# Kernel optimization log

Measured on AMD Instinct MI355X. Metric: run time of the kernel, lower is better.

## Reference

```python
import jax, jax.numpy as jnp
import numpy as np

KS = 3            # kernel_size
DILS = (1, 2, 4)  # dilation_list == padding_list
EPS = 1e-5        # BN eps


def _unfold3(x, d):
    # emulate F.unfold(kernel=3, dilation=d, padding=d, stride=1).view(b, c, 9, h, w)
    b, c, h, w = x.shape
    xp = jnp.pad(x, ((0, 0), (0, 0), (d, d), (d, d)))
    pats = [xp[:, :, i * d:i * d + h, j * d:j * d + w] for i in range(KS) for j in range(KS)]
    return jnp.stack(pats, axis=2)


def _conv1x1(x, w, b):
    return jnp.einsum('bchw,oc->bohw', x, w) + b[None, :, None, None]


def _bn_relu(x, g, be, m, v):
    s = g / jnp.sqrt(v + EPS)
    return jax.nn.relu(x * s[None, :, None, None] + (be - m * s)[None, :, None, None])


def _proj(x, w1, b1, g1, be1, m1, v1, w2, b2, g2, be2, m2, v2):
    h = _bn_relu(_conv1x1(x, w1, b1), g1, be1, m1, v1)
    return _bn_relu(_conv1x1(h, w2, b2), g2, be2, m2, v2)


def setup_inputs():
    key = jax.random.key(0)
    Cin, Ck, Cv, Cout = 512, 256, 256, 512
    B, H, W = 4, 64, 64
    ks = iter(jax.random.split(key, 48))

    def nrm(shape, s=0.02):
        return jax.random.normal(next(ks), shape, jnp.float32) * s

    def bn(c):
        return (jnp.ones((c,), jnp.float32) + nrm((c,), 0.1),  # gamma
                nrm((c,), 0.1),                                 # beta
                nrm((c,), 0.1),                                 # running mean
                jax.random.uniform(next(ks), (c,), jnp.float32, 0.5, 1.5))  # running var

    inp = {"x": jax.random.normal(next(ks), (B, Cin, H, W), jnp.float32)}
    for p in ("k", "q"):
        g1, be1, m1, v1 = bn(Ck)
        g2, be2, m2, v2 = bn(Ck)
        inp.update({
            p + "1_w": nrm((Ck, Cin)), p + "1_b": nrm((Ck,)),
            p + "1_g": g1, p + "1_be": be1, p + "1_m": m1, p + "1_v": v1,
            p + "2_w": nrm((Ck, Ck)), p + "2_b": nrm((Ck,)),
            p + "2_g": g2, p + "2_be": be2, p + "2_m": m2, p + "2_v": v2,
        })
    inp["v_w"] = nrm((Cv, Cin)); inp["v_b"] = nrm((Cv,))
    inp["w_w"] = nrm((Cout, Cv)); inp["w_b"] = nrm((Cout,))
    return inp


def reference(x,
              k1_w, k1_b, k1_g, k1_be, k1_m, k1_v,
              k2_w, k2_b, k2_g, k2_be, k2_m, k2_v,
              q1_w, q1_b, q1_g, q1_be, q1_m, q1_v,
              q2_w, q2_b, q2_g, q2_be, q2_m, q2_v,
              v_w, v_b, w_w, w_b):
    # scale == 1: MaxPool2d(1x1-equivalent) and final bilinear resize are identities.
    value = _conv1x1(x, v_w, v_b)                                  # (b,cv,h,w)
    keyf = _proj(x, k1_w, k1_b, k1_g, k1_be, k1_m, k1_v,
                 k2_w, k2_b, k2_g, k2_be, k2_m, k2_v)              # (b,ck,h,w)
    query = _proj(x, q1_w, q1_b, q1_g, q1_be, q1_m, q1_v,
                  q2_w, q2_b, q2_g, q2_be, q2_m, q2_v)             # (b,ck,h,w)
    uk = jnp.concatenate([_unfold3(keyf, d) for d in DILS], axis=2)   # (b,ck,27,h,w)
    uv = jnp.concatenate([_unfold3(value, d) for d in DILS], axis=2)  # (b,cv,27,h,w)
    sim = jnp.sum(uk * query[:, :, None], axis=1, keepdims=True)      # (b,1,27,h,w)
    sim = jax.nn.softmax(sim, axis=2)
    context = jnp.sum(sim * uv, axis=2)                               # (b,cv,h,w)
    return _conv1x1(context, w_w, w_b)
```

## Files before the change

kernel.cpp:

```cpp
#include <hip/hip_runtime.h>

#define HW   4096
#define Hh   64
#define Ww   64
#define NB   27
#define EPSBN 1e-5f

typedef _Float16 f16x8 __attribute__((ext_vector_type(8)));
typedef _Float16 f16x4 __attribute__((ext_vector_type(4)));
typedef _Float16 f16x2 __attribute__((ext_vector_type(2)));
typedef float    f32x4 __attribute__((ext_vector_type(4)));

__device__ __forceinline__ void gld_lds16(const void* g, void* l) {
    __builtin_amdgcn_global_load_lds(
        (const __attribute__((address_space(1))) unsigned int*)g,
        (__attribute__((address_space(3))) unsigned int*)l, 16, 0, 0);
}

struct GJob {
    const _Float16* in;
    const float*    xf;
    const float*    w;
    const float* b; const float* g; const float* be; const float* m; const float* v;
    _Float16* oh;
    float*    of;
};

__global__ __launch_bounds__(512, 2)
void gemm_f(GJob J0, GJob J1, GJob J2, int stage, int K, int JO, int mode)
{
    __shared__ _Float16 As[2][3][4096];
    __shared__ _Float16 Bs[2][16384];

    const int tid  = threadIdx.x;
    const int lane = tid & 63;
    const int w8   = tid >> 6;
    const int lr   = lane & 15;
    const int lg   = lane >> 4;
    const int wq   = w8 & 3;
    const int ph   = w8 >> 2;

    const int bid = blockIdx.x;
    const int xcd = bid & 7;
    const int jj  = bid >> 3;
    const int nb  = xcd * 8 + (jj >> 2);
    const int u   = jj & 3;

    const int nA = (stage == 1) ? 3 : 2;
    int js0, js1, js2, ob0, ob1, ob2;
    if (stage == 1)      { js0 = 0; js1 = 1; js2 = 2; ob0 = ob1 = ob2 = u * 64; }
    else if (stage == 2) { js0 = js1 = js2 = (u >> 1); ob0 = (u & 1) * 128; ob1 = ob0 + 64; ob2 = ob1; }
    else                 { js0 = js1 = js2 = 0; ob0 = u * 128; ob1 = ob0 + 64; ob2 = ob1; }

#define JSEL(js, f) ((js) == 0 ? J0.f : ((js) == 1 ? J1.f : J2.f))
    const float* w0 = JSEL(js0, w);
    const float* w1 = JSEL(js1, w);
    const float* w2 = JSEL(js2, w);
    const float* b0 = JSEL(js0, b); const float* g0 = JSEL(js0, g);
    const float* be0 = JSEL(js0, be); const float* m0 = JSEL(js0, m); const float* v0 = JSEL(js0, v);
    const float* b1 = JSEL(js1, b); const float* g1 = JSEL(js1, g);
    const float* be1 = JSEL(js1, be); const float* m1 = JSEL(js1, m); const float* v1 = JSEL(js1, v);
    const float* b2 = JSEL(js2, b); const float* g2 = JSEL(js2, g);
    const float* be2 = JSEL(js2, be); const float* m2 = JSEL(js2, m); const float* v2 = JSEL(js2, v);
    _Float16* oh0 = JSEL(js0, oh); float* of0 = JSEL(js0, of);
    _Float16* oh1 = JSEL(js1, oh); float* of1 = JSEL(js1, of);
    _Float16* oh2 = JSEL(js2, oh); float* of2 = JSEL(js2, of);
    const _Float16* bIn = JSEL(js0, in);
    const float*    bXf = JSEL(js0, xf);
#undef JSEL

    const int scol = (((lane & 7) ^ (lane >> 3)) << 3);
    const int rowA = w8 * 8 + (lane >> 3);
    const float* aS0 = w0 + (size_t)(ob0 + rowA) * K + scol;
    const float* aS1 = w1 + (size_t)(ob1 + rowA) * K + scol;
    const float* aS2 = w2 + (size_t)(ob2 + rowA) * K + scol;
    const int aoffW  = w8 * 1024 + lane * 16;

    const int rowB = w8 * 32 + (lane >> 3);
    const _Float16* bS = bIn ? (bIn + (size_t)(nb * 256 + rowB) * K + scol) : nullptr;

    const int px   = tid & 255;
    const int chh  = tid >> 8;
    const int pgS  = nb * 256 + px;
    const float* xbase = bXf ? (bXf + (size_t)(pgS >> 12) * 512 * HW + (pgS & 4095)) : nullptr;
    const int bxk  = (px & 7) << 4;
    const bool f32B = (bXf != nullptr);

    float fr[32];
    float ar0[8], ar1[8], ar2[8];

    auto ISSUE_A = [&](int rd) {
        const int kb = rd * 64;
        *(float4*)&ar0[0] = *(const float4*)(aS0 + kb);
        *(float4*)&ar0[4] = *(const float4*)(aS0 + kb + 4);
        *(float4*)&ar1[0] = *(const float4*)(aS1 + kb);
        *(float4*)&ar1[4] = *(const float4*)(aS1 + kb + 4);
        if (nA > 2) {
            *(float4*)&ar2[0] = *(const float4*)(aS2 + kb);
            *(float4*)&ar2[4] = *(const float4*)(aS2 + kb + 4);
        }
    };
    auto WRITE_A = [&](int buf) {
        f16x8 h0, h1, h2;
        #pragma unroll
        for (int i2 = 0; i2 < 8; ++i2) h0[i2] = (_Float16)ar0[i2];
        #pragma unroll
        for (int i2 = 0; i2 < 8; ++i2) h1[i2] = (_Float16)ar1[i2];
        *(f16x8*)((char*)&As[buf][0][0] + aoffW) = h0;
        *(f16x8*)((char*)&As[buf][1][0] + aoffW) = h1;
        if (nA > 2) {
            #pragma unroll
            for (int i2 = 0; i2 < 8; ++i2) h2[i2] = (_Float16)ar2[i2];
            *(f16x8*)((char*)&As[buf][2][0] + aoffW) = h2;
        }
    };
    auto ISSUE_BX = [&](int rd) {
        const int cb = rd * 64 + chh * 32;
        #pragma unroll
        for (int i2 = 0; i2 < 32; ++i2)
            fr[i2] = xbase[(size_t)(cb + i2) * HW];
    };
    auto WRITE_BX = [&](int buf) {
        #pragma unroll
        for (int g4 = 0; g4 < 4; ++g4) {
            f16x8 hv;
            #pragma unroll
            for (int i2 = 0; i2 < 8; ++i2) hv[i2] = (_Float16)fr[g4 * 8 + i2];
            *(f16x8*)((char*)&Bs[buf][0] + px * 128 + ((chh * 64 + g4 * 16) ^ bxk)) = hv;
        }
    };
    auto STAGE_B16 = [&](int buf, int rd) {
        const int kb = rd * 64;
        #pragma unroll
        for (int j2 = 0; j2 < 4; ++j2)
            gld_lds16(bS + (size_t)j2 * 8 * K + kb, (char*)&Bs[buf][0] + w8 * 4096 + j2 * 1024);
    };

    f32x4 acc0[8] = {}, acc1[8] = {}, acc2[8] = {};
    const int nr = K >> 6;

    ISSUE_A(0);
    if (f32B) { ISSUE_BX(0); WRITE_BX(0); }
    else      { STAGE_B16(0, 0); }
    WRITE_A(0);
    __syncthreads();

    int cur = 0;
    for (int rd = 0; rd < nr; ++rd) {
        const bool more = (rd + 1 < nr);
        if (more) {
            ISSUE_A(rd + 1);
            if (f32B) ISSUE_BX(rd + 1);
            else      STAGE_B16(cur ^ 1, rd + 1);
        }

        #pragma unroll
        for (int ks = 0; ks < 2; ++ks) {
            const int colx = (ks * 64 + lg * 16) ^ ((lr & 7) << 4);
            f16x8 bfr[8];
            #pragma unroll
            for (int t = 0; t < 8; ++t)
                bfr[t] = *(const f16x8*)((const char*)&Bs[cur][0] + (ph * 128 + t * 16 + lr) * 128 + colx);
            const int aoff = (wq * 16 + lr) * 128 + colx;
            const f16x8 af0 = *(const f16x8*)((const char*)&As[cur][0][0] + aoff);
            const f16x8 af1 = *(const f16x8*)((const char*)&As[cur][1][0] + aoff);
            #pragma unroll
            for (int t = 0; t < 8; ++t)
                acc0[t] = __builtin_amdgcn_mfma_f32_16x16x32_f16(af0, bfr[t], acc0[t], 0, 0, 0);
            #pragma unroll
            for (int t = 0; t < 8; ++t)
                acc1[t] = __builtin_amdgcn_mfma_f32_16x16x32_f16(af1, bfr[t], acc1[t], 0, 0, 0);
            if (nA > 2) {
                const f16x8 af2 = *(const f16x8*)((const char*)&As[cur][2][0] + aoff);
                #pragma unroll
                for (int t = 0; t < 8; ++t)
                    acc2[t] = __builtin_amdgcn_mfma_f32_16x16x32_f16(af2, bfr[t], acc2[t], 0, 0, 0);
            }
        }

        if (more) {
            WRITE_A(cur ^ 1);
            if (f32B) WRITE_BX(cur ^ 1);
        }
        __syncthreads();
        cur ^= 1;
    }

#define EPI(accS, obS, bS_, gS, beS, mS, vS, ohS, ofS) do {                      \
        const int o4 = (obS) + wq * 16 + lg * 4;                                 \
        float sc[4], off[4];                                                     \
        _Pragma("unroll")                                                        \
        for (int r = 0; r < 4; ++r) {                                            \
            const int o = o4 + r;                                                \
            if (gS) { float s = (gS)[o] * rsqrtf((vS)[o] + EPSBN);               \
                      sc[r] = s; off[r] = fmaf((bS_)[o] - (mS)[o], s, (beS)[o]); }\
            else    { sc[r] = 1.f; off[r] = (bS_)[o]; }                          \
        }                                                                        \
        _Pragma("unroll")                                                        \
        for (int t = 0; t < 8; ++t) {                                            \
            const int pg = nb * 256 + ph * 128 + t * 16 + lr;                    \
            float vv[4];                                                         \
            _Pragma("unroll")                                                    \
            for (int r = 0; r < 4; ++r) {                                        \
                float tv = fmaf(accS[t][r], sc[r], off[r]);                      \
                vv[r] = (gS) ? fmaxf(tv, 0.f) : tv;                              \
            }                                                                    \
            if (mode == 0) {                                                     \
                f16x4 hh;                                                        \
                _Pragma("unroll")                                                \
                for (int r = 0; r < 4; ++r) hh[r] = (_Float16)vv[r];             \
                *(f16x4*)((ohS) + (size_t)pg * JO + o4) = hh;                    \
            } else {                                                             \
                _Pragma("unroll")                                                \
                for (int r = 0; r < 4; ++r)                                      \
                    (ofS)[((size_t)(pg >> 12) * JO + o4 + r) * HW + (pg & 4095)] = vv[r]; \
            }                                                                    \
        }                                                                        \
    } while (0)

    EPI(acc0, ob0, b0, g0, be0, m0, v0, oh0, of0);
    EPI(acc1, ob1, b1, g1, be1, m1, v1, oh1, of1);
    if (nA > 2) EPI(acc2, ob2, b2, g2, be2, m2, v2, oh2, of2);
#undef EPI
}

__global__ __launch_bounds__(256)
void attn_fused(const _Float16* __restrict__ keyT, const _Float16* __restrict__ qryT,
                const _Float16* __restrict__ valT, _Float16* __restrict__ ctxT)
{
    const int tid  = threadIdx.x;
    const int slot = tid & 31;
    const int b    = blockIdx.y;
    const int p    = blockIdx.x * 8 + (tid >> 5);
    const int y    = p >> 6;
    const int xc   = p & 63;

    int   idx[NB];
    float valf[NB];
    #pragma unroll
    for (int n = 0; n < NB; ++n) {
        const int d  = (n < 9) ? 1 : (n < 18 ? 2 : 4);
        const int i  = (n / 3) % 3 - 1;
        const int j  = n % 3 - 1;
        const int yy = y + i * d, xx = xc + j * d;
        const bool ok = ((unsigned)yy < (unsigned)Hh) && ((unsigned)xx < (unsigned)Ww);
        idx[n]  = min(max(yy, 0), Hh - 1) * Ww + min(max(xx, 0), Ww - 1);
        valf[n] = ok ? 1.f : 0.f;
    }

    const size_t base = (size_t)b * HW * 256 + slot * 8;
    const f16x8 q8 = *(const f16x8*)(qryT + base + (size_t)p * 256);

    f16x2 qp[4];
    qp[0] = __builtin_shufflevector(q8, q8, 0, 1);
    qp[1] = __builtin_shufflevector(q8, q8, 2, 3);
    qp[2] = __builtin_shufflevector(q8, q8, 4, 5);
    qp[3] = __builtin_shufflevector(q8, q8, 6, 7);

    float sim[NB];
    #pragma unroll
    for (int n = 0; n < NB; ++n) {
        const f16x8 k8 = *(const f16x8*)(keyT + base + (size_t)idx[n] * 256);
        float s = 0.f;
        s = __builtin_amdgcn_fdot2(__builtin_shufflevector(k8, k8, 0, 1), qp[0], s, false);
        s = __builtin_amdgcn_fdot2(__builtin_shufflevector(k8, k8, 2, 3), qp[1], s, false);
        s = __builtin_amdgcn_fdot2(__builtin_shufflevector(k8, k8, 4, 5), qp[2], s, false);
        s = __builtin_amdgcn_fdot2(__builtin_shufflevector(k8, k8, 6, 7), qp[3], s, false);
        sim[n] = s;
    }

    #pragma unroll
    for (int n = 0; n < NB; ++n) {
        float s = sim[n];
        s += __shfl_xor(s, 1);
        s += __shfl_xor(s, 2);
        s += __shfl_xor(s, 4);
        s += __shfl_xor(s, 8);
        s += __shfl_xor(s, 16);
        sim[n] = s * valf[n];
    }

    float mx = sim[0];
    #pragma unroll
    for (int n = 1; n < NB; ++n) mx = fmaxf(mx, sim[n]);
    float sum = 0.f;
    #pragma unroll
    for (int n = 0; n < NB; ++n) { sim[n] = __expf(sim[n] - mx); sum += sim[n]; }
    const float inv = 1.f / sum;
    #pragma unroll
    for (int n = 0; n < NB; ++n) sim[n] = sim[n] * inv * valf[n];

    float acc[8];
    #pragma unroll
    for (int i = 0; i < 8; ++i) acc[i] = 0.f;
    #pragma unroll
    for (int n = 0; n < NB; ++n) {
        const f16x8 v8 = *(const f16x8*)(valT + base + (size_t)idx[n] * 256);
        const float w = sim[n];
        #pragma unroll
        for (int i = 0; i < 8; ++i) acc[i] = fmaf(w, (float)v8[i], acc[i]);
    }

    f16x8 h;
    #pragma unroll
    for (int i = 0; i < 8; ++i) h[i] = (_Float16)acc[i];
    *(f16x8*)(ctxT + base + (size_t)p * 256) = h;
}

extern "C" void kernel_launch(void* const* d_in, const int* in_sizes, int n_in,
                              void* d_out, int out_size, void* d_ws, size_t ws_size,
                              hipStream_t stream)
{
    (void)in_sizes; (void)n_in; (void)out_size; (void)ws_size;
    const float* x     = (const float*)d_in[0];
    const float* k1_w  = (const float*)d_in[1];
    const float* k1_b  = (const float*)d_in[2];
    const float* k1_g  = (const float*)d_in[3];
    const float* k1_be = (const float*)d_in[4];
    const float* k1_m  = (const float*)d_in[5];
    const float* k1_v  = (const float*)d_in[6];
    const float* k2_w  = (const float*)d_in[7];
    const float* k2_b  = (const float*)d_in[8];
    const float* k2_g  = (const float*)d_in[9];
    const float* k2_be = (const float*)d_in[10];
    const float* k2_m  = (const float*)d_in[11];
    const float* k2_v  = (const float*)d_in[12];
    const float* q1_w  = (const float*)d_in[13];
    const float* q1_b  = (const float*)d_in[14];
    const float* q1_g  = (const float*)d_in[15];
    const float* q1_be = (const float*)d_in[16];
    const float* q1_m  = (const float*)d_in[17];
    const float* q1_v  = (const float*)d_in[18];
    const float* q2_w  = (const float*)d_in[19];
    const float* q2_b  = (const float*)d_in[20];
    const float* q2_g  = (const float*)d_in[21];
    const float* q2_be = (const float*)d_in[22];
    const float* q2_m  = (const float*)d_in[23];
    const float* q2_v  = (const float*)d_in[24];
    const float* v_w   = (const float*)d_in[25];
    const float* v_b   = (const float*)d_in[26];
    const float* w_w   = (const float*)d_in[27];
    const float* w_b   = (const float*)d_in[28];

    _Float16* hw = (_Float16*)d_ws;
    const size_t SH = (size_t)4 * HW * 256;
    _Float16* k1T   = hw;
    _Float16* q1T   = k1T + SH;
    _Float16* valT  = q1T + SH;
    _Float16* ctxT  = valT + SH;
    _Float16* keyPC = ctxT + SH;
    _Float16* qryPC = keyPC + SH;

    GJob jv  = { nullptr, x, v_w,  v_b,  nullptr, nullptr, nullptr, nullptr, valT,  nullptr };
    GJob jk1 = { nullptr, x, k1_w, k1_b, k1_g, k1_be, k1_m, k1_v,            k1T,   nullptr };
    GJob jq1 = { nullptr, x, q1_w, q1_b, q1_g, q1_be, q1_m, q1_v,            q1T,   nullptr };
    GJob jk2 = { k1T, nullptr, k2_w, k2_b, k2_g, k2_be, k2_m, k2_v,          keyPC, nullptr };
    GJob jq2 = { q1T, nullptr, q2_w, q2_b, q2_g, q2_be, q2_m, q2_v,          qryPC, nullptr };
    GJob jw  = { ctxT, nullptr, w_w, w_b,  nullptr, nullptr, nullptr, nullptr, nullptr, (float*)d_out };

    gemm_f<<<256, 512, 0, stream>>>(jv, jk1, jq1, 1, 512, 256, 0);
    gemm_f<<<256, 512, 0, stream>>>(jk2, jq2, jq2, 2, 256, 256, 0);
    attn_fused<<<dim3(512, 4), 256, 0, stream>>>(keyPC, qryPC, valT, ctxT);
    gemm_f<<<256, 512, 0, stream>>>(jw, jw, jw, 4, 256, 512, 2);
}
```

Before: 86.96 us.

## Deepen fp32 B-operand prefetch to two tiles with register double buffering

For the fp32-input GEMM path, the loop now keeps two register buffers for the strided x loads and issues the loads two K-tiles ahead. It uses explicit vmcnt waits and raw s_barrier in place of __syncthreads, so in-flight loads can cross the barrier. Launch bounds drop to one block per CU so the extra 32 registers of prefetch state fit. The aim is to hide the high latency of the strided global loads, at the cost of lower occupancy and fragile hand-written waitcnt counts.

```diff
diff --git a/kernel.cpp b/kernel.cpp
--- a/kernel.cpp
+++ b/kernel.cpp
@@ -26,7 +26,7 @@
     float*    of;
 };
 
-__global__ __launch_bounds__(512, 2)
+__global__ __launch_bounds__(512, 1)
 void gemm_f(GJob J0, GJob J1, GJob J2, int stage, int K, int JO, int mode)
 {
     __shared__ _Float16 As[2][3][4096];
@@ -86,7 +86,6 @@
     const int bxk  = (px & 7) << 4;
     const bool f32B = (bXf != nullptr);
 
-    float fr[32];
     float ar0[8], ar1[8], ar2[8];
 
     auto ISSUE_A = [&](int rd) {
@@ -114,21 +113,6 @@
             *(f16x8*)((char*)&As[buf][2][0] + aoffW) = h2;
         }
     };
-    auto ISSUE_BX = [&](int rd) {
-        const int cb = rd * 64 + chh * 32;
-        #pragma unroll
-        for (int i2 = 0; i2 < 32; ++i2)
-            fr[i2] = xbase[(size_t)(cb + i2) * HW];
-    };
-    auto WRITE_BX = [&](int buf) {
-        #pragma unroll
-        for (int g4 = 0; g4 < 4; ++g4) {
-            f16x8 hv;
-            #pragma unroll
-            for (int i2 = 0; i2 < 8; ++i2) hv[i2] = (_Float16)fr[g4 * 8 + i2];
-            *(f16x8*)((char*)&Bs[buf][0] + px * 128 + ((chh * 64 + g4 * 16) ^ bxk)) = hv;
-        }
-    };
     auto STAGE_B16 = [&](int buf, int rd) {
         const int kb = rd * 64;
         #pragma unroll
@@ -136,24 +120,26 @@
             gld_lds16(bS + (size_t)j2 * 8 * K + kb, (char*)&Bs[buf][0] + w8 * 4096 + j2 * 1024);
     };
 
+#define ISSUE_BXM(RD, FR) do {                                                 \
+        const int cb_ = (RD) * 64 + chh * 32;                                  \
+        _Pragma("unroll")                                                      \
+        for (int i2 = 0; i2 < 32; ++i2)                                        \
+            FR[i2] = xbase[(size_t)(cb_ + i2) * HW];                           \
+    } while (0)
+#define WRITE_BXM(BUF, FR) do {                                                \
+        _Pragma("unroll")                                                      \
+        for (int g4 = 0; g4 < 4; ++g4) {                                       \
+            f16x8 hv;                                                          \
+            _Pragma("unroll")                                                  \
+            for (int i2 = 0; i2 < 8; ++i2) hv[i2] = (_Float16)FR[g4 * 8 + i2]; \
+            *(f16x8*)((char*)&Bs[BUF][0] + px * 128 + ((chh * 64 + g4 * 16) ^ bxk)) = hv; \
+        }                                                                      \
+    } while (0)
+
     f32x4 acc0[8] = {}, acc1[8] = {}, acc2[8] = {};
     const int nr = K >> 6;
 
-    ISSUE_A(0);
-    if (f32B) { ISSUE_BX(0); WRITE_BX(0); }
-    else      { STAGE_B16(0, 0); }
-    WRITE_A(0);
-    __syncthreads();
-
-    int cur = 0;
-    for (int rd = 0; rd < nr; ++rd) {
-        const bool more = (rd + 1 < nr);
-        if (more) {
-            ISSUE_A(rd + 1);
-            if (f32B) ISSUE_BX(rd + 1);
-            else      STAGE_B16(cur ^ 1, rd + 1);
-        }
-
+    auto MFMA_TILE = [&](int cur) {
         #pragma unroll
         for (int ks = 0; ks < 2; ++ks) {
             const int colx = (ks * 64 + lg * 16) ^ ((lr & 7) << 4);
@@ -177,13 +163,57 @@
                     acc2[t] = __builtin_amdgcn_mfma_f32_16x16x32_f16(af2, bfr[t], acc2[t], 0, 0, 0);
             }
         }
-
-        if (more) {
-            WRITE_A(cur ^ 1);
-            if (f32B) WRITE_BX(cur ^ 1);
-        }
+    };
+
+    if (f32B) {
+        float frA[32], frB[32];
+        int cur = 0;
+        ISSUE_A(0);
+        ISSUE_BXM(0, frA);
+        asm volatile("s_waitcnt vmcnt(0)" ::: "memory");
+        WRITE_A(0);
+        WRITE_BXM(0, frA);
+        ISSUE_BXM(1, frA);
+        asm volatile("s_waitcnt lgkmcnt(0)" ::: "memory");
+        __builtin_amdgcn_s_barrier();
+        __builtin_amdgcn_sched_barrier(0);
+
+#define TILE_BODY(RD, FRIN, FROUT) do {                                        \
+            const bool m1_ = (RD) + 1 < nr, m2_ = (RD) + 2 < nr;               \
+            if (m1_) ISSUE_A((RD) + 1);                                        \
+            if (m2_) ISSUE_BXM((RD) + 2, FROUT);                               \
+            MFMA_TILE(cur);                                                    \
+            if (m2_) asm volatile("s_waitcnt vmcnt(32)" ::: "memory");         \
+            else     asm volatile("s_waitcnt vmcnt(0)"  ::: "memory");         \
+            if (m1_) { WRITE_A(cur ^ 1); WRITE_BXM(cur ^ 1, FRIN); }           \
+            asm volatile("s_waitcnt lgkmcnt(0)" ::: "memory");                 \
+            __builtin_amdgcn_s_barrier();                                      \
+            __builtin_amdgcn_sched_barrier(0);                                 \
+            cur ^= 1;                                                          \
+        } while (0)
+
+        for (int rd = 0; rd < nr; rd += 2) {
+            TILE_BODY(rd, frA, frB);
+            TILE_BODY(rd + 1, frB, frA);
+        }
+#undef TILE_BODY
+    } else {
+        ISSUE_A(0);
+        STAGE_B16(0, 0);
+        WRITE_A(0);
         __syncthreads();
-        cur ^= 1;
+        int cur = 0;
+        for (int rd = 0; rd < nr; ++rd) {
+            const bool more = (rd + 1 < nr);
+            if (more) {
+                ISSUE_A(rd + 1);
+                STAGE_B16(cur ^ 1, rd + 1);
+            }
+            MFMA_TILE(cur);
+            if (more) WRITE_A(cur ^ 1);
+            __syncthreads();
+            cur ^= 1;
+        }
     }
 
 #define EPI(accS, obS, bS_, gS, beS, mS, vS, ohS, ofS) do {                      \
```

New measurement: 330.5 us. 280% more time.

## Triple-buffer fp16 B tiles with async LDS loads and explicit waitcnt barriers

Applied to the files above, without the earlier changes.

For the fp16-input GEMM path, the B operand moves to a three-deep LDS ring filled by global_load_lds two rounds ahead, synchronised with hand-placed s_waitcnt vmcnt plus s_barrier instead of __syncthreads. Deeper prefetch is meant to hide global-load latency behind the MFMA work. The larger shared buffer forces launch bounds down to one 512-thread block per CU, which costs occupancy. The fp32-input path keeps its double-buffer schedule.

```diff
diff --git a/kernel.cpp b/kernel.cpp
--- a/kernel.cpp
+++ b/kernel.cpp
@@ -26,11 +26,11 @@
     float*    of;
 };
 
-__global__ __launch_bounds__(512, 2)
+__global__ __launch_bounds__(512, 1)
 void gemm_f(GJob J0, GJob J1, GJob J2, int stage, int K, int JO, int mode)
 {
     __shared__ _Float16 As[2][3][4096];
-    __shared__ _Float16 Bs[2][16384];
+    __shared__ _Float16 Bs[3][16384];
 
     const int tid  = threadIdx.x;
     const int lane = tid & 63;
@@ -86,8 +86,8 @@
     const int bxk  = (px & 7) << 4;
     const bool f32B = (bXf != nullptr);
 
+    float ar0[8], ar1[8], ar2[8];
     float fr[32];
-    float ar0[8], ar1[8], ar2[8];
 
     auto ISSUE_A = [&](int rd) {
         const int kb = rd * 64;
@@ -139,31 +139,17 @@
     f32x4 acc0[8] = {}, acc1[8] = {}, acc2[8] = {};
     const int nr = K >> 6;
 
-    ISSUE_A(0);
-    if (f32B) { ISSUE_BX(0); WRITE_BX(0); }
-    else      { STAGE_B16(0, 0); }
-    WRITE_A(0);
-    __syncthreads();
-
-    int cur = 0;
-    for (int rd = 0; rd < nr; ++rd) {
-        const bool more = (rd + 1 < nr);
-        if (more) {
-            ISSUE_A(rd + 1);
-            if (f32B) ISSUE_BX(rd + 1);
-            else      STAGE_B16(cur ^ 1, rd + 1);
-        }
-
+    auto MFMA_TILE = [&](int bb, int ab) {
         #pragma unroll
         for (int ks = 0; ks < 2; ++ks) {
             const int colx = (ks * 64 + lg * 16) ^ ((lr & 7) << 4);
             f16x8 bfr[8];
             #pragma unroll
             for (int t = 0; t < 8; ++t)
-                bfr[t] = *(const f16x8*)((const char*)&Bs[cur][0] + (ph * 128 + t * 16 + lr) * 128 + colx);
+                bfr[t] = *(const f16x8*)((const char*)&Bs[bb][0] + (ph * 128 + t * 16 + lr) * 128 + colx);
             const int aoff = (wq * 16 + lr) * 128 + colx;
-            const f16x8 af0 = *(const f16x8*)((const char*)&As[cur][0][0] + aoff);
-            const f16x8 af1 = *(const f16x8*)((const char*)&As[cur][1][0] + aoff);
+            const f16x8 af0 = *(const f16x8*)((const char*)&As[ab][0][0] + aoff);
+            const f16x8 af1 = *(const f16x8*)((const char*)&As[ab][1][0] + aoff);
             #pragma unroll
             for (int t = 0; t < 8; ++t)
                 acc0[t] = __builtin_amdgcn_mfma_f32_16x16x32_f16(af0, bfr[t], acc0[t], 0, 0, 0);
@@ -171,19 +157,56 @@
             for (int t = 0; t < 8; ++t)
                 acc1[t] = __builtin_amdgcn_mfma_f32_16x16x32_f16(af1, bfr[t], acc1[t], 0, 0, 0);
             if (nA > 2) {
-                const f16x8 af2 = *(const f16x8*)((const char*)&As[cur][2][0] + aoff);
+                const f16x8 af2 = *(const f16x8*)((const char*)&As[ab][2][0] + aoff);
                 #pragma unroll
                 for (int t = 0; t < 8; ++t)
                     acc2[t] = __builtin_amdgcn_mfma_f32_16x16x32_f16(af2, bfr[t], acc2[t], 0, 0, 0);
             }
         }
-
-        if (more) {
-            WRITE_A(cur ^ 1);
-            if (f32B) WRITE_BX(cur ^ 1);
-        }
+    };
+
+    if (f32B) {
+        ISSUE_A(0);
+        ISSUE_BX(0);
+        WRITE_BX(0);
+        WRITE_A(0);
         __syncthreads();
-        cur ^= 1;
+        int cur = 0;
+        for (int rd = 0; rd < nr; ++rd) {
+            const bool more = (rd + 1 < nr);
+            if (more) {
+                ISSUE_A(rd + 1);
+                ISSUE_BX(rd + 1);
+            }
+            MFMA_TILE(cur, cur);
+            if (more) {
+                WRITE_A(cur ^ 1);
+                WRITE_BX(cur ^ 1);
+            }
+            __syncthreads();
+            cur ^= 1;
+        }
+    } else {
+        STAGE_B16(0, 0);
+        ISSUE_A(0);
+        STAGE_B16(1, 1);
+        WRITE_A(0);
+        asm volatile("s_waitcnt vmcnt(4) lgkmcnt(0)" ::: "memory");
+        __builtin_amdgcn_s_barrier();
+        __builtin_amdgcn_sched_barrier(0);
+
+        for (int rd = 0; rd < nr; ++rd) {
+            const bool m1 = (rd + 1 < nr);
+            const bool m2 = (rd + 2 < nr);
+            if (m1) ISSUE_A(rd + 1);
+            if (m2) STAGE_B16((rd + 2) % 3, rd + 2);
+            MFMA_TILE(rd % 3, rd & 1);
+            if (m1) WRITE_A((rd + 1) & 1);
+            if (m2) asm volatile("s_waitcnt vmcnt(4) lgkmcnt(0)" ::: "memory");
+            else    asm volatile("s_waitcnt vmcnt(0) lgkmcnt(0)" ::: "memory");
+            __builtin_amdgcn_s_barrier();
+            __builtin_amdgcn_sched_barrier(0);
+        }
     }
 
 #define EPI(accS, obS, bS_, gS, beS, mS, vS, ohS, ofS) do {                      \
```

New measurement: 84.32 us. -3.0%, faster.
